# Kernel optimization log

Hardware: AMD Instinct MI355X
Metric: run time of the kernel (lower is better)

Reference implementation:

```python
import jax, jax.numpy as jnp
import numpy as np

B, E, N = 8, 256, 32          # triples, padded edges per triple, neighbors per edge
D, RD = 512, 768              # graph_dim, relation-semantic dim
R = 2000                      # num relations
L = 2                         # relation-context layers
K = 8                         # top_k neighbor similarity
M, HEADS = 32, 8              # memory tokens, memory-attention heads
HLLM = 4096                   # llm hidden size
EPS = 1e-5


def _ln(x, g, b):
    mu = jnp.mean(x, -1, keepdims=True)
    var = jnp.mean(jnp.square(x - mu), -1, keepdims=True)
    return (x - mu) * jax.lax.rsqrt(var + EPS) * g + b


def setup_inputs() -> dict:
    key = jax.random.key(0)
    ks = iter(jax.random.split(key, 40))
    nrm = lambda shape, s=0.02: jax.random.normal(next(ks), shape, jnp.float32) * s
    return {
        'edge_rel_ids': jax.random.randint(next(ks), (B, E), 0, R, jnp.int32),
        'neighbor_rel_ids': jax.random.randint(next(ks), (B, E, N), 0, R, jnp.int32),
        'edge_mask': jnp.ones((B, E), jnp.float32),
        'rel_emb': nrm((R, RD), 1.0),
        'rp_w': nrm((D, RD)), 'rp_b': jnp.zeros((D,), jnp.float32),
        'ly_vw': nrm((L, D, D)), 'ly_vb': jnp.zeros((L, D), jnp.float32),
        'ly_ow': nrm((L, D, D)), 'ly_ob': jnp.zeros((L, D), jnp.float32),
        'ly_n1g': jnp.ones((L, D), jnp.float32), 'ly_n1b': jnp.zeros((L, D), jnp.float32),
        'ly_n2g': jnp.ones((L, D), jnp.float32), 'ly_n2b': jnp.zeros((L, D), jnp.float32),
        'ly_w1': nrm((L, 4 * D, D)), 'ly_b1': jnp.zeros((L, 4 * D), jnp.float32),
        'ly_w2': nrm((L, D, 4 * D)), 'ly_b2': jnp.zeros((L, D), jnp.float32),
        'mem_q': nrm((M, D)),
        't_qw': nrm((D, D)), 't_qb': jnp.zeros((D,), jnp.float32),
        't_kw': nrm((D, D)), 't_kb': jnp.zeros((D,), jnp.float32),
        't_vw': nrm((D, D)), 't_vb': jnp.zeros((D,), jnp.float32),
        't_ow': nrm((D, D)), 't_ob': jnp.zeros((D,), jnp.float32),
        'proj_w': nrm((HLLM, D)), 'proj_b': jnp.zeros((HLLM,), jnp.float32),
    }


def reference(edge_rel_ids, neighbor_rel_ids, edge_mask, rel_emb, rp_w, rp_b,
              ly_vw, ly_vb, ly_ow, ly_ob, ly_n1g, ly_n1b, ly_n2g, ly_n2b,
              ly_w1, ly_b1, ly_w2, ly_b2, mem_q,
              t_qw, t_qb, t_kw, t_kb, t_vw, t_vb, t_ow, t_ob, proj_w, proj_b):
    rel_vector = lambda ids: rel_emb[ids] @ rp_w.T + rp_b  # embedding gather + rel_proj
    rel_vec = rel_vector(edge_rel_ids)            # [B,E,D]
    neigh = rel_vector(neighbor_rel_ids)          # [B,E,N,D] dominant gather traffic
    # per-edge cosine similarity to neighbor relations, top-k mean aggregation
    rn = rel_vec / jnp.maximum(jnp.linalg.norm(rel_vec, axis=-1, keepdims=True), 1e-12)
    nn_ = neigh / jnp.maximum(jnp.linalg.norm(neigh, axis=-1, keepdims=True), 1e-12)
    sims = jnp.einsum('bend,bed->ben', nn_, rn)   # [B,E,N]
    _, top_idx = jax.lax.top_k(sims, K)           # [B,E,K]
    agg = jnp.take_along_axis(neigh, top_idx[..., None], axis=2).mean(axis=2)  # [B,E,D]
    # RelationContextLayer stack. Each layer attends from one edge-state token to a
    # single context token: softmax over one key is identically 1, so the MHA
    # reduces exactly to out_proj(v_proj(context)) -- same math as torch MHA here.
    states = rel_vec
    for l in range(L):
        attn = (agg @ ly_vw[l].T + ly_vb[l]) @ ly_ow[l].T + ly_ob[l]
        states = _ln(states + attn, ly_n1g[l], ly_n1b[l])
        ff = jax.nn.gelu(states @ ly_w1[l].T + ly_b1[l], approximate=False) @ ly_w2[l].T + ly_b2[l]
        states = _ln(states + ff, ly_n2g[l], ly_n2b[l])
        states = states * edge_mask[..., None]
    # GraphMemoryTokenizer: learned queries cross-attend over padded edge states
    dh = D // HEADS
    q = (mem_q @ t_qw.T + t_qb).reshape(M, HEADS, dh)
    k = (states @ t_kw.T + t_kb).reshape(B, E, HEADS, dh)
    v = (states @ t_vw.T + t_vb).reshape(B, E, HEADS, dh)
    scores = jnp.einsum('mhd,behd->bhme', q, k) / jnp.sqrt(jnp.asarray(dh, q.dtype))
    scores = jnp.where(edge_mask[:, None, None, :] == 0, jnp.finfo(scores.dtype).min, scores)
    attnw = jax.nn.softmax(scores, axis=-1)
    mem = jnp.einsum('bhme,behd->bmhd', attnw, v).reshape(B, M, D)
    mem = mem @ t_ow.T + t_ob
    no_edges = jnp.sum(edge_mask, axis=1) == 0    # rows with zero edges -> zero memory
    mem = jnp.where(no_edges[:, None, None], 0.0, mem)
    return mem @ proj_w.T + proj_b                # [B,M,HLLM]
```

## Files before the change

kernel.cpp:

```cpp
#include <hip/hip_runtime.h>
#include <hip/hip_bf16.h>
#include <math.h>

#define B_   8
#define E_   256
#define N_   32
#define D_   512
#define RD_  768
#define R_   2000
#define L_   2
#define K_   8
#define M_   32
#define H_   8
#define DH_  64
#define HL_  4096

typedef float f32x4 __attribute__((ext_vector_type(4)));
typedef __bf16 bf16x8 __attribute__((ext_vector_type(8)));
typedef const __attribute__((address_space(1))) void GVoid;
typedef __attribute__((address_space(3))) void LVoid;

__device__ __forceinline__ float gelu_exact(float x) {
    return 0.5f * x * (1.0f + erff(x * 0.70710678118654752f));
}
__device__ __forceinline__ unsigned short f2bf(float x) {
    return __hip_bfloat16_raw(__float2bfloat16(x)).x;
}

template <int TM, int TN, int ACT_GELU, int OUT_BF16, int HAS_BIAS, int FLAGS>
__global__ __launch_bounds__(256) void gemm_mfma(const unsigned short* __restrict__ A,
                                                 const unsigned short* __restrict__ W,
                                                 const float* __restrict__ bias,
                                                 void* __restrict__ Cv,
                                                 int M, int N, int K,
                                                 size_t sA, size_t sW, size_t sC,
                                                 const float* __restrict__ rowflag) {
    constexpr int WTM = TM / 2, WTN = TN / 2;
    constexpr int RM = WTM / 16, RN = WTN / 16;
    constexpr int AI = TM / 32;
    constexpr int BI = TN / 32;
    __shared__ __align__(16) unsigned short As[TM * 64];
    __shared__ __align__(16) unsigned short Bs[TN * 64];

    const size_t z = blockIdx.z;
    A += z * sA; W += z * sW;

    const int tid = threadIdx.x;
    const int wave = tid >> 6, lane = tid & 63;
    const int quad = lane >> 4, l16 = lane & 15;
    const int wm = wave >> 1, wn = wave & 1;
    const int bm = blockIdx.y * TM, bn = blockIdx.x * TN;

    const int sub = lane >> 3;
    const int cpr = (lane & 7) ^ sub;

    f32x4 acc[RM][RN];
#pragma unroll
    for (int i = 0; i < RM; i++)
#pragma unroll
        for (int j = 0; j < RN; j++) acc[i][j] = (f32x4){0.f, 0.f, 0.f, 0.f};

    for (int k0 = 0; k0 < K; k0 += 64) {
        __syncthreads();
#pragma unroll
        for (int i = 0; i < AI; i++) {
            int r0 = (wave * AI + i) * 8;
            const unsigned short* g = A + (size_t)(bm + r0 + sub) * K + k0 + cpr * 8;
            __builtin_amdgcn_global_load_lds((GVoid*)g, (LVoid*)&As[r0 * 64], 16, 0, 0);
        }
#pragma unroll
        for (int i = 0; i < BI; i++) {
            int r0 = (wave * BI + i) * 8;
            const unsigned short* g = W + (size_t)(bn + r0 + sub) * K + k0 + cpr * 8;
            __builtin_amdgcn_global_load_lds((GVoid*)g, (LVoid*)&Bs[r0 * 64], 16, 0, 0);
        }
        __syncthreads();

#pragma unroll
        for (int h = 0; h < 2; h++) {
            bf16x8 af[RM], bf[RN];
#pragma unroll
            for (int i = 0; i < RM; i++) {
                int r = wm * WTM + i * 16 + l16;
                int ch = (h * 4 + quad) ^ (r & 7);
                af[i] = *(const bf16x8*)&As[r * 64 + ch * 8];
            }
#pragma unroll
            for (int j = 0; j < RN; j++) {
                int r = wn * WTN + j * 16 + l16;
                int ch = (h * 4 + quad) ^ (r & 7);
                bf[j] = *(const bf16x8*)&Bs[r * 64 + ch * 8];
            }
#pragma unroll
            for (int i = 0; i < RM; i++)
#pragma unroll
                for (int j = 0; j < RN; j++)
                    acc[i][j] = __builtin_amdgcn_mfma_f32_16x16x32_bf16(af[i], bf[j], acc[i][j], 0, 0, 0);
        }
    }

#pragma unroll
    for (int i = 0; i < RM; i++) {
#pragma unroll
        for (int j = 0; j < RN; j++) {
            int c = bn + wn * WTN + j * 16 + l16;
            float bv = HAS_BIAS ? bias[c] : 0.f;
#pragma unroll
            for (int reg = 0; reg < 4; reg++) {
                int r = bm + wm * WTM + i * 16 + quad * 4 + reg;
                if (r < M) {
                    float v = acc[i][j][reg] + bv;
                    if (ACT_GELU) v = gelu_exact(v);
                    if (FLAGS) v *= rowflag[r >> 5];
                    if (OUT_BF16)
                        ((unsigned short*)(Cv))[z * sC + (size_t)r * N + c] = f2bf(v);
                    else
                        ((float*)(Cv))[z * sC + (size_t)r * N + c] = v;
                }
            }
        }
    }
}

struct PrepArgs {
    const float* src[9];
    unsigned short* dst[9];
    int cum4[10];
    int nb_cvt, nb_tr, nb_bf, total4;
    const float* ly_vw; unsigned short* vwT;
    const float* ly_ow; const float* ly_vb; const float* ly_ob; float* bfuse;
    const float* t_kb; const float* t_vb; float* kvb;
    const float* edge_mask; float* flags;
    const float* mem_q; const float* t_qw; const float* t_qb; float* qbuf;
};

__global__ __launch_bounds__(256) void prep_all(PrepArgs a) {
    int bx = blockIdx.x, tid = threadIdx.x;
    if (bx < a.nb_cvt) {
        int i = bx * 256 + tid;
        if (i < a.total4) {
            int k = 0;
#pragma unroll
            for (int j = 0; j < 8; j++) if (i >= a.cum4[j + 1]) k = j + 1;
            int o = i - a.cum4[k];
            float4 v = ((const float4*)a.src[k])[o];
            ushort4 u;
            u.x = f2bf(v.x); u.y = f2bf(v.y); u.z = f2bf(v.z); u.w = f2bf(v.w);
            ((ushort4*)a.dst[k])[o] = u;
        }
        return;
    }
    bx -= a.nb_cvt;
    if (bx < a.nb_tr) {
        __shared__ float tile[32][33];
        int l = bx >> 8, t16 = bx & 255;
        int j0 = (t16 >> 4) * 32, k0 = (t16 & 15) * 32;
        int tx = tid & 31, ty = tid >> 5;
        const float* src = a.ly_vw + (size_t)l * 512 * 512;
        for (int r = ty; r < 32; r += 8)
            tile[r][tx] = src[(size_t)(j0 + r) * 512 + k0 + tx];
        __syncthreads();
        unsigned short* dst = a.vwT + (size_t)l * 512 * 512;
        for (int r = ty; r < 32; r += 8)
            dst[(size_t)(k0 + r) * 512 + j0 + tx] = f2bf(tile[tx][r]);
        return;
    }
    bx -= a.nb_tr;
    if (bx < a.nb_bf) {
        int wid = bx * 4 + (tid >> 6);
        int z = wid >> 9, n = wid & 511, lane = tid & 63;
        const float* owr = a.ly_ow + (size_t)z * 512 * 512 + (size_t)n * 512;
        const float* vbr = a.ly_vb + (size_t)z * 512;
        float s = 0.f;
#pragma unroll
        for (int j = 0; j < 8; j++) s += owr[lane + 64 * j] * vbr[lane + 64 * j];
#pragma unroll
        for (int off = 32; off; off >>= 1) s += __shfl_xor(s, off, 64);
        if (lane == 0) a.bfuse[z * 512 + n] = s + a.ly_ob[z * 512 + n];
        return;
    }
    bx -= a.nb_bf;
    if (bx < 1) {
        for (int n = tid; n < 512; n += 256) {
            a.kvb[n] = a.t_kb[n];
            a.kvb[n + 512] = a.t_vb[n];
        }
        __shared__ float red[4];
        for (int b = 0; b < B_; b++) {
            float s = a.edge_mask[b * E_ + tid];
#pragma unroll
            for (int off = 32; off; off >>= 1) s += __shfl_xor(s, off, 64);
            if ((tid & 63) == 0) red[tid >> 6] = s;
            __syncthreads();
            if (tid == 0)
                a.flags[b] = (red[0] + red[1] + red[2] + red[3] == 0.f) ? 0.f : 1.f;
            __syncthreads();
        }
        return;
    }
    bx -= 1;
    {
        int wid = bx * 4 + (tid >> 6);
        int m = wid >> 9, n = wid & 511, lane = tid & 63;
        const float* ar = a.mem_q + (size_t)m * 512;
        const float* br = a.t_qw + (size_t)n * 512;
        float s = 0.f;
#pragma unroll
        for (int j = 0; j < 8; j++) s += ar[lane + 64 * j] * br[lane + 64 * j];
#pragma unroll
        for (int off = 32; off; off >>= 1) s += __shfl_xor(s, off, 64);
        if (lane == 0) a.qbuf[(size_t)m * 512 + n] = s + a.t_qb[n];
    }
}

__global__ void sim_topk_agg(const int* __restrict__ eids, const int* __restrict__ nids,
                             const float* __restrict__ proj,
                             unsigned short* __restrict__ agg_bf, float* __restrict__ states) {
    int be = blockIdx.x, tid = threadIdx.x;
    __shared__ float ev[512];
    __shared__ float sims[32];
    __shared__ int nid_s[32];
    __shared__ int sel[8];

    int eid = eids[be];
    const float* ep = proj + (size_t)eid * D_;
    float e0 = ep[tid], e1 = ep[tid + 256];
    ev[tid] = e0; ev[tid + 256] = e1;
    states[(size_t)be * D_ + tid] = e0;
    states[(size_t)be * D_ + tid + 256] = e1;
    if (tid < 32) nid_s[tid] = nids[be * N_ + tid];
    __syncthreads();

    int wid = tid >> 6, lane = tid & 63;
    float se = 0.f;
#pragma unroll
    for (int j = 0; j < 8; j++) { float v = ev[lane + 64 * j]; se += v * v; }
#pragma unroll
    for (int off = 32; off; off >>= 1) se += __shfl_xor(se, off, 64);
    float en = fmaxf(sqrtf(se), 1e-12f);

    for (int n = wid; n < N_; n += 4) {
        int nid = nid_s[n];
        const float* np = proj + (size_t)nid * D_;
        float s = 0.f, s2 = 0.f;
#pragma unroll
        for (int j = 0; j < 8; j++) {
            float v = np[lane + 64 * j];
            s += v * ev[lane + 64 * j];
            s2 += v * v;
        }
#pragma unroll
        for (int off = 32; off; off >>= 1) {
            s += __shfl_xor(s, off, 64);
            s2 += __shfl_xor(s2, off, 64);
        }
        if (lane == 0) sims[n] = s / (fmaxf(sqrtf(s2), 1e-12f) * en);
    }
    __syncthreads();

    if (tid == 0) {
        unsigned used = 0;
        for (int k = 0; k < K_; k++) {
            float best = -3.402823466e38f; int bi = 0;
            for (int n = 0; n < N_; n++)
                if (!((used >> n) & 1u) && sims[n] > best) { best = sims[n]; bi = n; }
            used |= 1u << bi;
            sel[k] = nid_s[bi];
        }
    }
    __syncthreads();

    float a0 = 0.f, a1 = 0.f;
#pragma unroll
    for (int k = 0; k < K_; k++) {
        const float* sp = proj + (size_t)sel[k] * D_;
        a0 += sp[tid]; a1 += sp[tid + 256];
    }
    agg_bf[(size_t)be * D_ + tid] = f2bf(a0 * 0.125f);
    agg_bf[(size_t)be * D_ + tid + 256] = f2bf(a1 * 0.125f);
}

__global__ void add_ln_kernel(const float* __restrict__ x, const float* __restrict__ y,
                              int ystride, const float* __restrict__ g,
                              const float* __restrict__ bb, const float* __restrict__ mask,
                              float* __restrict__ out, unsigned short* __restrict__ out_bf) {
    int t = blockIdx.x, tid = threadIdx.x;
    const float* xr = x + (size_t)t * D_;
    const float* yr = y + (size_t)t * ystride;
    float x0 = xr[tid] + yr[tid];
    float x1 = xr[tid + 256] + yr[tid + 256];
    __shared__ float red[8];
    float s = x0 + x1;
#pragma unroll
    for (int off = 32; off; off >>= 1) s += __shfl_xor(s, off, 64);
    int wid = tid >> 6;
    if ((tid & 63) == 0) red[wid] = s;
    __syncthreads();
    float mean = (red[0] + red[1] + red[2] + red[3]) * (1.f / 512.f);
    float d0 = x0 - mean, d1 = x1 - mean;
    float v = d0 * d0 + d1 * d1;
#pragma unroll
    for (int off = 32; off; off >>= 1) v += __shfl_xor(v, off, 64);
    if ((tid & 63) == 0) red[4 + wid] = v;
    __syncthreads();
    float var = (red[4] + red[5] + red[6] + red[7]) * (1.f / 512.f);
    float rs = rsqrtf(var + 1e-5f);
    float mv = mask ? mask[t] : 1.f;
    float o0 = (d0 * rs * g[tid] + bb[tid]) * mv;
    float o1 = (d1 * rs * g[tid + 256] + bb[tid + 256]) * mv;
    out[(size_t)t * D_ + tid] = o0;
    out[(size_t)t * D_ + tid + 256] = o1;
    out_bf[(size_t)t * D_ + tid] = f2bf(o0);
    out_bf[(size_t)t * D_ + tid + 256] = f2bf(o1);
}

__global__ void mem_attn(const float* __restrict__ qb, const float* __restrict__ kv,
                         const float* __restrict__ mask, unsigned short* __restrict__ memb) {
    int idx = blockIdx.x;
    int b = idx & 7;
    int h = (idx >> 3) & 7;
    int m = idx >> 6;
    int tid = threadIdx.x;
    __shared__ float qh[64];
    __shared__ float sc[256];
    __shared__ float red[8];
    __shared__ float oacc[4][64];

    float mk = mask[b * E_ + tid];
    if (tid < 64) qh[tid] = qb[m * D_ + h * DH_ + tid];
    __syncthreads();
    const float* kr = kv + ((size_t)(b * E_ + tid)) * 1024 + h * DH_;
    float s = 0.f;
#pragma unroll
    for (int d = 0; d < DH_; d += 4) {
        float4 k4 = *(const float4*)(kr + d);
        s += k4.x * qh[d] + k4.y * qh[d + 1] + k4.z * qh[d + 2] + k4.w * qh[d + 3];
    }
    s *= 0.125f;
    if (mk == 0.f) s = -3.402823466e38f;
    float mx = s;
#pragma unroll
    for (int off = 32; off; off >>= 1) mx = fmaxf(mx, __shfl_xor(mx, off, 64));
    if ((tid & 63) == 0) red[tid >> 6] = mx;
    __syncthreads();
    mx = fmaxf(fmaxf(red[0], red[1]), fmaxf(red[2], red[3]));
    float p = expf(s - mx);
    float sum = p;
#pragma unroll
    for (int off = 32; off; off >>= 1) sum += __shfl_xor(sum, off, 64);
    if ((tid & 63) == 0) red[4 + (tid >> 6)] = sum;
    __syncthreads();
    sum = red[4] + red[5] + red[6] + red[7];
    sc[tid] = p / sum;
    __syncthreads();
    int d = tid & 63, part = tid >> 6;
    const float* vcol = kv + ((size_t)(b * E_ + part * 64)) * 1024 + 512 + h * DH_ + d;
    float acc = 0.f;
#pragma unroll 8
    for (int e = 0; e < 64; e++) acc += sc[part * 64 + e] * vcol[(size_t)e * 1024];
    oacc[part][d] = acc;
    __syncthreads();
    if (part == 0)
        memb[((size_t)(b * M_ + m)) * D_ + h * DH_ + d] =
            f2bf(oacc[0][d] + oacc[1][d] + oacc[2][d] + oacc[3][d]);
}

extern "C" void kernel_launch(void* const* d_in, const int* in_sizes, int n_in,
                              void* d_out, int out_size, void* d_ws, size_t ws_size,
                              hipStream_t stream) {
    const int*   edge_rel_ids     = (const int*)d_in[0];
    const int*   neighbor_rel_ids = (const int*)d_in[1];
    const float* edge_mask        = (const float*)d_in[2];
    const float* rel_emb          = (const float*)d_in[3];
    const float* rp_w             = (const float*)d_in[4];
    const float* rp_b             = (const float*)d_in[5];
    const float* ly_vw            = (const float*)d_in[6];
    const float* ly_vb            = (const float*)d_in[7];
    const float* ly_ow            = (const float*)d_in[8];
    const float* ly_ob            = (const float*)d_in[9];
    const float* ly_n1g           = (const float*)d_in[10];
    const float* ly_n1b           = (const float*)d_in[11];
    const float* ly_n2g           = (const float*)d_in[12];
    const float* ly_n2b           = (const float*)d_in[13];
    const float* ly_w1            = (const float*)d_in[14];
    const float* ly_b1            = (const float*)d_in[15];
    const float* ly_w2            = (const float*)d_in[16];
    const float* ly_b2            = (const float*)d_in[17];
    const float* mem_q            = (const float*)d_in[18];
    const float* t_qw             = (const float*)d_in[19];
    const float* t_qb             = (const float*)d_in[20];
    const float* t_kw             = (const float*)d_in[21];
    const float* t_kb             = (const float*)d_in[22];
    const float* t_vw             = (const float*)d_in[23];
    const float* t_vb             = (const float*)d_in[24];
    const float* t_ow             = (const float*)d_in[25];
    const float* t_ob             = (const float*)d_in[26];
    const float* proj_w           = (const float*)d_in[27];
    const float* proj_b           = (const float*)d_in[28];
    float* out = (float*)d_out;
    (void)ws_size; (void)in_sizes; (void)n_in; (void)out_size;

    char* ws = (char*)d_ws;
    size_t off = 0;
    auto allocf = [&](size_t n) { float* p = (float*)(ws + off); off += ((n * 4 + 255) & ~(size_t)255); return p; };
    auto allocb = [&](size_t n) { unsigned short* p = (unsigned short*)(ws + off); off += ((n * 2 + 255) & ~(size_t)255); return p; };

    const int T = B_ * E_;

    float* proj    = allocf((size_t)R_ * D_);
    float* states  = allocf((size_t)T * D_);
    float* tmpB    = allocf((size_t)T * D_);
    float* attnall = allocf((size_t)T * 2 * D_);
    float* qbuf    = allocf((size_t)M_ * D_);
    float* bfuse   = allocf(2 * D_);
    float* kvb     = allocf(2 * D_);
    float* flags   = allocf(B_);
    float* kvbuf   = attnall;

    unsigned short* rel_bf    = allocb((size_t)2048 * RD_);
    unsigned short* rpw_bf    = allocb((size_t)D_ * RD_);
    unsigned short* agg_bf    = allocb((size_t)T * D_);
    unsigned short* states_bf = allocb((size_t)T * D_);
    unsigned short* ff1_bf    = allocb((size_t)T * 4 * D_);
    unsigned short* vwT_bf    = allocb((size_t)L_ * D_ * D_);
    unsigned short* ow_bf     = allocb((size_t)L_ * D_ * D_);
    unsigned short* wfuse_bf  = allocb((size_t)L_ * D_ * D_);
    unsigned short* w1_bf     = allocb((size_t)L_ * 4 * D_ * D_);
    unsigned short* w2_bf     = allocb((size_t)L_ * 4 * D_ * D_);
    unsigned short* kvw_bf    = allocb((size_t)2 * D_ * D_);
    unsigned short* tow_bf    = allocb((size_t)D_ * D_);
    unsigned short* pw_bf     = allocb((size_t)HL_ * D_);
    unsigned short* memb_bf   = allocb((size_t)B_ * M_ * D_);
    unsigned short* mem2_bf   = allocb((size_t)B_ * M_ * D_);

    PrepArgs a;
    int sizes[9] = { R_ * RD_, D_ * RD_, L_ * D_ * D_, L_ * 4 * D_ * D_,
                     L_ * 4 * D_ * D_, D_ * D_, D_ * D_, D_ * D_, HL_ * D_ };
    const float* srcs[9] = { rel_emb, rp_w, ly_ow, ly_w1, ly_w2, t_kw, t_vw, t_ow, proj_w };
    unsigned short* dsts[9] = { rel_bf, rpw_bf, ow_bf, w1_bf, w2_bf,
                                kvw_bf, kvw_bf + (size_t)D_ * D_, tow_bf, pw_bf };
    int cum = 0;
    for (int i = 0; i < 9; i++) {
        a.src[i] = srcs[i]; a.dst[i] = dsts[i];
        a.cum4[i] = cum; cum += sizes[i] / 4;
    }
    a.cum4[9] = cum;
    a.total4 = cum;
    a.nb_cvt = (cum + 255) / 256;
    a.nb_tr = 512;
    a.nb_bf = 256;
    a.ly_vw = ly_vw; a.vwT = vwT_bf;
    a.ly_ow = ly_ow; a.ly_vb = ly_vb; a.ly_ob = ly_ob; a.bfuse = bfuse;
    a.t_kb = t_kb; a.t_vb = t_vb; a.kvb = kvb;
    a.edge_mask = edge_mask; a.flags = flags;
    a.mem_q = mem_q; a.t_qw = t_qw; a.t_qb = t_qb; a.qbuf = qbuf;
    int nblk = a.nb_cvt + a.nb_tr + a.nb_bf + 1 + 4096;
    prep_all<<<nblk, 256, 0, stream>>>(a);

    gemm_mfma<32, 64, 0, 0, 1, 0><<<dim3(D_ / 64, 64), 256, 0, stream>>>(
        rel_bf, rpw_bf, rp_b, proj, R_, D_, RD_, 0, 0, 0, nullptr);
    sim_topk_agg<<<T, 256, 0, stream>>>(edge_rel_ids, neighbor_rel_ids, proj,
                                        agg_bf, states);

    gemm_mfma<32, 64, 0, 1, 0, 0><<<dim3(8, 16, 2), 256, 0, stream>>>(
        ow_bf, vwT_bf, nullptr, wfuse_bf, D_, D_, D_,
        (size_t)D_ * D_, (size_t)D_ * D_, (size_t)D_ * D_, nullptr);
    gemm_mfma<64, 64, 0, 0, 1, 0><<<dim3(2 * D_ / 64, T / 64), 256, 0, stream>>>(
        agg_bf, wfuse_bf, bfuse, attnall, T, 2 * D_, D_, 0, 0, 0, nullptr);

    for (int l = 0; l < L_; l++) {
        add_ln_kernel<<<T, 256, 0, stream>>>(states, attnall + (size_t)l * D_, 2 * D_,
                                             ly_n1g + l * D_, ly_n1b + l * D_, nullptr,
                                             states, states_bf);
        gemm_mfma<64, 64, 1, 1, 1, 0><<<dim3(4 * D_ / 64, T / 64), 256, 0, stream>>>(
            states_bf, w1_bf + (size_t)l * 4 * D_ * D_, ly_b1 + l * 4 * D_,
            ff1_bf, T, 4 * D_, D_, 0, 0, 0, nullptr);
        gemm_mfma<32, 64, 0, 0, 1, 0><<<dim3(D_ / 64, T / 32), 256, 0, stream>>>(
            ff1_bf, w2_bf + (size_t)l * 4 * D_ * D_, ly_b2 + l * D_,
            tmpB, T, D_, 4 * D_, 0, 0, 0, nullptr);
        add_ln_kernel<<<T, 256, 0, stream>>>(states, tmpB, D_,
                                             ly_n2g + l * D_, ly_n2b + l * D_, edge_mask,
                                             states, states_bf);
    }

    gemm_mfma<64, 64, 0, 0, 1, 0><<<dim3(2 * D_ / 64, T / 64), 256, 0, stream>>>(
        states_bf, kvw_bf, kvb, kvbuf, T, 2 * D_, D_, 0, 0, 0, nullptr);

    mem_attn<<<B_ * M_ * H_, 256, 0, stream>>>(qbuf, kvbuf, edge_mask, memb_bf);

    gemm_mfma<32, 64, 0, 1, 1, 1><<<dim3(D_ / 64, 8), 256, 0, stream>>>(
        memb_bf, tow_bf, t_ob, mem2_bf, B_ * M_, D_, D_, 0, 0, 0, flags);

    gemm_mfma<32, 64, 0, 0, 1, 0><<<dim3(HL_ / 64, 8), 256, 0, stream>>>(
        mem2_bf, pw_bf, proj_b, out, B_ * M_, HL_, D_, 0, 0, 0, nullptr);
}
```

Before: 322.1 us.

## Fuse all stages into one persistent cooperative kernel with grid syncs

```diff
diff --git a/kernel.cpp b/kernel.cpp
--- a/kernel.cpp
+++ b/kernel.cpp
@@ -1,6 +1,9 @@
 #include <hip/hip_runtime.h>
+#include <hip/hip_cooperative_groups.h>
 #include <hip/hip_bf16.h>
 #include <math.h>
+
+namespace cg = cooperative_groups;
 
 #define B_   8
 #define E_   256
@@ -27,115 +30,130 @@
     return __hip_bfloat16_raw(__float2bfloat16(x)).x;
 }
 
-template <int TM, int TN, int ACT_GELU, int OUT_BF16, int HAS_BIAS, int FLAGS>
-__global__ __launch_bounds__(256) void gemm_mfma(const unsigned short* __restrict__ A,
-                                                 const unsigned short* __restrict__ W,
-                                                 const float* __restrict__ bias,
-                                                 void* __restrict__ Cv,
-                                                 int M, int N, int K,
-                                                 size_t sA, size_t sW, size_t sC,
-                                                 const float* __restrict__ rowflag) {
-    constexpr int WTM = TM / 2, WTN = TN / 2;
-    constexpr int RM = WTM / 16, RN = WTN / 16;
-    constexpr int AI = TM / 32;
-    constexpr int BI = TN / 32;
-    __shared__ __align__(16) unsigned short As[TM * 64];
-    __shared__ __align__(16) unsigned short Bs[TN * 64];
-
-    const size_t z = blockIdx.z;
-    A += z * sA; W += z * sW;
-
-    const int tid = threadIdx.x;
-    const int wave = tid >> 6, lane = tid & 63;
-    const int quad = lane >> 4, l16 = lane & 15;
-    const int wm = wave >> 1, wn = wave & 1;
-    const int bm = blockIdx.y * TM, bn = blockIdx.x * TN;
-
-    const int sub = lane >> 3;
-    const int cpr = (lane & 7) ^ sub;
-
-    f32x4 acc[RM][RN];
-#pragma unroll
-    for (int i = 0; i < RM; i++)
-#pragma unroll
-        for (int j = 0; j < RN; j++) acc[i][j] = (f32x4){0.f, 0.f, 0.f, 0.f};
-
-    for (int k0 = 0; k0 < K; k0 += 64) {
-        __syncthreads();
-#pragma unroll
-        for (int i = 0; i < AI; i++) {
-            int r0 = (wave * AI + i) * 8;
-            const unsigned short* g = A + (size_t)(bm + r0 + sub) * K + k0 + cpr * 8;
-            __builtin_amdgcn_global_load_lds((GVoid*)g, (LVoid*)&As[r0 * 64], 16, 0, 0);
-        }
-#pragma unroll
-        for (int i = 0; i < BI; i++) {
-            int r0 = (wave * BI + i) * 8;
-            const unsigned short* g = W + (size_t)(bn + r0 + sub) * K + k0 + cpr * 8;
-            __builtin_amdgcn_global_load_lds((GVoid*)g, (LVoid*)&Bs[r0 * 64], 16, 0, 0);
-        }
-        __syncthreads();
-
-#pragma unroll
-        for (int h = 0; h < 2; h++) {
-            bf16x8 af[RM], bf[RN];
-#pragma unroll
-            for (int i = 0; i < RM; i++) {
-                int r = wm * WTM + i * 16 + l16;
-                int ch = (h * 4 + quad) ^ (r & 7);
-                af[i] = *(const bf16x8*)&As[r * 64 + ch * 8];
-            }
-#pragma unroll
-            for (int j = 0; j < RN; j++) {
-                int r = wn * WTN + j * 16 + l16;
-                int ch = (h * 4 + quad) ^ (r & 7);
-                bf[j] = *(const bf16x8*)&Bs[r * 64 + ch * 8];
-            }
-#pragma unroll
-            for (int i = 0; i < RM; i++)
-#pragma unroll
-                for (int j = 0; j < RN; j++)
-                    acc[i][j] = __builtin_amdgcn_mfma_f32_16x16x32_bf16(af[i], bf[j], acc[i][j], 0, 0, 0);
-        }
-    }
-
-#pragma unroll
-    for (int i = 0; i < RM; i++) {
-#pragma unroll
-        for (int j = 0; j < RN; j++) {
-            int c = bn + wn * WTN + j * 16 + l16;
-            float bv = HAS_BIAS ? bias[c] : 0.f;
-#pragma unroll
-            for (int reg = 0; reg < 4; reg++) {
-                int r = bm + wm * WTM + i * 16 + quad * 4 + reg;
-                if (r < M) {
-                    float v = acc[i][j][reg] + bv;
-                    if (ACT_GELU) v = gelu_exact(v);
-                    if (FLAGS) v *= rowflag[r >> 5];
-                    if (OUT_BF16)
-                        ((unsigned short*)(Cv))[z * sC + (size_t)r * N + c] = f2bf(v);
-                    else
-                        ((float*)(Cv))[z * sC + (size_t)r * N + c] = v;
-                }
-            }
-        }
-    }
-}
-
-struct PrepArgs {
-    const float* src[9];
-    unsigned short* dst[9];
-    int cum4[10];
-    int nb_cvt, nb_tr, nb_bf, total4;
+struct AllArgs {
+    const float* csrc[9]; unsigned short* cdst[9]; int cum4[10];
+    int nb_cvt, total4, nb_prep;
     const float* ly_vw; unsigned short* vwT;
     const float* ly_ow; const float* ly_vb; const float* ly_ob; float* bfuse;
     const float* t_kb; const float* t_vb; float* kvb;
     const float* edge_mask; float* flags;
     const float* mem_q; const float* t_qw; const float* t_qb; float* qbuf;
+    const int* eids; const int* nids;
+    unsigned short* rel_bf; unsigned short* rpw_bf; const float* rp_b; float* proj;
+    unsigned short* agg_bf; float* states; unsigned short* states_bf;
+    unsigned short* ow_bf; unsigned short* wfuse;
+    float* attnall;
+    const float* n1g; const float* n1b; const float* n2g; const float* n2b;
+    unsigned short* w1; const float* b1; unsigned short* w2; const float* b2;
+    unsigned short* ff1; float* tmpB;
+    unsigned short* kvw; float* kvbuf;
+    unsigned short* membf; unsigned short* toww; const float* t_ob; unsigned short* mem2;
+    unsigned short* pw; const float* proj_b; float* outp;
 };
 
-__global__ __launch_bounds__(256) void prep_all(PrepArgs a) {
-    int bx = blockIdx.x, tid = threadIdx.x;
+template <int TM, int TN, int GELU_, int OBF_, int BIAS_, int FLAGS_>
+__device__ __forceinline__ void gemm_stage(const unsigned short* __restrict__ A,
+                                           const unsigned short* __restrict__ W,
+                                           const float* __restrict__ bias,
+                                           void* __restrict__ Cv,
+                                           int M, int N, int K,
+                                           const float* __restrict__ rowflag,
+                                           int zn, size_t sA, size_t sW, size_t sC,
+                                           unsigned char* SM) {
+    constexpr int WTM = TM / 2, WTN = TN / 2;
+    constexpr int RM = WTM / 16, RN = WTN / 16;
+    constexpr int AI = TM / 32, BI = TN / 32;
+    unsigned short* As = (unsigned short*)SM;
+    unsigned short* Bs = (unsigned short*)(SM + 8192);
+
+    const int tid = threadIdx.x;
+    const int wave = tid >> 6, lane = tid & 63;
+    const int quad = lane >> 4, l16 = lane & 15;
+    const int wm = wave >> 1, wn = wave & 1;
+    const int sub = lane >> 3;
+    const int cpr = (lane & 7) ^ sub;
+    const int ntx = N / TN;
+    const int nty = (M + TM - 1) / TM;
+    const int ntiles = ntx * nty * zn;
+
+    for (int t0 = blockIdx.x; t0 < ntiles; t0 += gridDim.x) {
+        int z = t0 / (ntx * nty);
+        int tt = t0 - z * (ntx * nty);
+        int bn = (tt % ntx) * TN, bm = (tt / ntx) * TM;
+        const unsigned short* Az = A + (size_t)z * sA;
+        const unsigned short* Wz = W + (size_t)z * sW;
+
+        f32x4 acc[RM][RN];
+#pragma unroll
+        for (int i = 0; i < RM; i++)
+#pragma unroll
+            for (int j = 0; j < RN; j++) acc[i][j] = (f32x4){0.f, 0.f, 0.f, 0.f};
+
+        for (int k0 = 0; k0 < K; k0 += 64) {
+            __syncthreads();
+#pragma unroll
+            for (int i = 0; i < AI; i++) {
+                int r0 = (wave * AI + i) * 8;
+                const unsigned short* g = Az + (size_t)(bm + r0 + sub) * K + k0 + cpr * 8;
+                __builtin_amdgcn_global_load_lds((GVoid*)g, (LVoid*)&As[r0 * 64], 16, 0, 0);
+            }
+#pragma unroll
+            for (int i = 0; i < BI; i++) {
+                int r0 = (wave * BI + i) * 8;
+                const unsigned short* g = Wz + (size_t)(bn + r0 + sub) * K + k0 + cpr * 8;
+                __builtin_amdgcn_global_load_lds((GVoid*)g, (LVoid*)&Bs[r0 * 64], 16, 0, 0);
+            }
+            __syncthreads();
+
+#pragma unroll
+            for (int h = 0; h < 2; h++) {
+                bf16x8 af[RM], bf[RN];
+#pragma unroll
+                for (int i = 0; i < RM; i++) {
+                    int r = wm * WTM + i * 16 + l16;
+                    int ch = (h * 4 + quad) ^ (r & 7);
+                    af[i] = *(const bf16x8*)&As[r * 64 + ch * 8];
+                }
+#pragma unroll
+                for (int j = 0; j < RN; j++) {
+                    int r = wn * WTN + j * 16 + l16;
+                    int ch = (h * 4 + quad) ^ (r & 7);
+                    bf[j] = *(const bf16x8*)&Bs[r * 64 + ch * 8];
+                }
+#pragma unroll
+                for (int i = 0; i < RM; i++)
+#pragma unroll
+                    for (int j = 0; j < RN; j++)
+                        acc[i][j] = __builtin_amdgcn_mfma_f32_16x16x32_bf16(af[i], bf[j], acc[i][j], 0, 0, 0);
+            }
+        }
+
+#pragma unroll
+        for (int i = 0; i < RM; i++) {
+#pragma unroll
+            for (int j = 0; j < RN; j++) {
+                int c = bn + wn * WTN + j * 16 + l16;
+                float bv = BIAS_ ? bias[c] : 0.f;
+#pragma unroll
+                for (int reg = 0; reg < 4; reg++) {
+                    int r = bm + wm * WTM + i * 16 + quad * 4 + reg;
+                    if (r < M) {
+                        float v = acc[i][j][reg] + bv;
+                        if (GELU_) v = gelu_exact(v);
+                        if (FLAGS_) v *= rowflag[r >> 5];
+                        if (OBF_)
+                            ((unsigned short*)Cv)[(size_t)z * sC + (size_t)r * N + c] = f2bf(v);
+                        else
+                            ((float*)Cv)[(size_t)z * sC + (size_t)r * N + c] = v;
+                    }
+                }
+            }
+        }
+    }
+}
+
+__device__ __forceinline__ void prep_unit(const AllArgs& a, int bx, unsigned char* SM) {
+    int tid = threadIdx.x;
     if (bx < a.nb_cvt) {
         int i = bx * 256 + tid;
         if (i < a.total4) {
@@ -143,30 +161,30 @@
 #pragma unroll
             for (int j = 0; j < 8; j++) if (i >= a.cum4[j + 1]) k = j + 1;
             int o = i - a.cum4[k];
-            float4 v = ((const float4*)a.src[k])[o];
+            float4 v = ((const float4*)a.csrc[k])[o];
             ushort4 u;
             u.x = f2bf(v.x); u.y = f2bf(v.y); u.z = f2bf(v.z); u.w = f2bf(v.w);
-            ((ushort4*)a.dst[k])[o] = u;
+            ((ushort4*)a.cdst[k])[o] = u;
         }
         return;
     }
     bx -= a.nb_cvt;
-    if (bx < a.nb_tr) {
-        __shared__ float tile[32][33];
+    if (bx < 512) {
+        float* tile = (float*)SM;
         int l = bx >> 8, t16 = bx & 255;
         int j0 = (t16 >> 4) * 32, k0 = (t16 & 15) * 32;
         int tx = tid & 31, ty = tid >> 5;
         const float* src = a.ly_vw + (size_t)l * 512 * 512;
         for (int r = ty; r < 32; r += 8)
-            tile[r][tx] = src[(size_t)(j0 + r) * 512 + k0 + tx];
+            tile[r * 33 + tx] = src[(size_t)(j0 + r) * 512 + k0 + tx];
         __syncthreads();
         unsigned short* dst = a.vwT + (size_t)l * 512 * 512;
         for (int r = ty; r < 32; r += 8)
-            dst[(size_t)(k0 + r) * 512 + j0 + tx] = f2bf(tile[tx][r]);
+            dst[(size_t)(k0 + r) * 512 + j0 + tx] = f2bf(tile[tx * 33 + r]);
         return;
     }
-    bx -= a.nb_tr;
-    if (bx < a.nb_bf) {
+    bx -= 512;
+    if (bx < 256) {
         int wid = bx * 4 + (tid >> 6);
         int z = wid >> 9, n = wid & 511, lane = tid & 63;
         const float* owr = a.ly_ow + (size_t)z * 512 * 512 + (size_t)n * 512;
@@ -179,13 +197,13 @@
         if (lane == 0) a.bfuse[z * 512 + n] = s + a.ly_ob[z * 512 + n];
         return;
     }
-    bx -= a.nb_bf;
+    bx -= 256;
     if (bx < 1) {
+        float* red = (float*)SM;
         for (int n = tid; n < 512; n += 256) {
             a.kvb[n] = a.t_kb[n];
             a.kvb[n + 512] = a.t_vb[n];
         }
-        __shared__ float red[4];
         for (int b = 0; b < B_; b++) {
             float s = a.edge_mask[b * E_ + tid];
 #pragma unroll
@@ -213,22 +231,20 @@
     }
 }
 
-__global__ void sim_topk_agg(const int* __restrict__ eids, const int* __restrict__ nids,
-                             const float* __restrict__ proj,
-                             unsigned short* __restrict__ agg_bf, float* __restrict__ states) {
-    int be = blockIdx.x, tid = threadIdx.x;
-    __shared__ float ev[512];
-    __shared__ float sims[32];
-    __shared__ int nid_s[32];
-    __shared__ int sel[8];
-
-    int eid = eids[be];
-    const float* ep = proj + (size_t)eid * D_;
+__device__ __forceinline__ void topk_unit(const AllArgs& a, int be, unsigned char* SM) {
+    int tid = threadIdx.x;
+    float* ev = (float*)SM;
+    float* sims = (float*)(SM + 2048);
+    int* nid_s = (int*)(SM + 2176);
+    int* sel = (int*)(SM + 2304);
+
+    int eid = a.eids[be];
+    const float* ep = a.proj + (size_t)eid * D_;
     float e0 = ep[tid], e1 = ep[tid + 256];
     ev[tid] = e0; ev[tid + 256] = e1;
-    states[(size_t)be * D_ + tid] = e0;
-    states[(size_t)be * D_ + tid + 256] = e1;
-    if (tid < 32) nid_s[tid] = nids[be * N_ + tid];
+    a.states[(size_t)be * D_ + tid] = e0;
+    a.states[(size_t)be * D_ + tid + 256] = e1;
+    if (tid < 32) nid_s[tid] = a.nids[be * N_ + tid];
     __syncthreads();
 
     int wid = tid >> 6, lane = tid & 63;
@@ -241,7 +257,7 @@
 
     for (int n = wid; n < N_; n += 4) {
         int nid = nid_s[n];
-        const float* np = proj + (size_t)nid * D_;
+        const float* np = a.proj + (size_t)nid * D_;
         float s = 0.f, s2 = 0.f;
 #pragma unroll
         for (int j = 0; j < 8; j++) {
@@ -273,96 +289,179 @@
     float a0 = 0.f, a1 = 0.f;
 #pragma unroll
     for (int k = 0; k < K_; k++) {
-        const float* sp = proj + (size_t)sel[k] * D_;
+        const float* sp = a.proj + (size_t)sel[k] * D_;
         a0 += sp[tid]; a1 += sp[tid + 256];
     }
-    agg_bf[(size_t)be * D_ + tid] = f2bf(a0 * 0.125f);
-    agg_bf[(size_t)be * D_ + tid + 256] = f2bf(a1 * 0.125f);
-}
-
-__global__ void add_ln_kernel(const float* __restrict__ x, const float* __restrict__ y,
-                              int ystride, const float* __restrict__ g,
-                              const float* __restrict__ bb, const float* __restrict__ mask,
-                              float* __restrict__ out, unsigned short* __restrict__ out_bf) {
-    int t = blockIdx.x, tid = threadIdx.x;
-    const float* xr = x + (size_t)t * D_;
-    const float* yr = y + (size_t)t * ystride;
-    float x0 = xr[tid] + yr[tid];
-    float x1 = xr[tid + 256] + yr[tid + 256];
-    __shared__ float red[8];
-    float s = x0 + x1;
-#pragma unroll
-    for (int off = 32; off; off >>= 1) s += __shfl_xor(s, off, 64);
-    int wid = tid >> 6;
-    if ((tid & 63) == 0) red[wid] = s;
-    __syncthreads();
-    float mean = (red[0] + red[1] + red[2] + red[3]) * (1.f / 512.f);
-    float d0 = x0 - mean, d1 = x1 - mean;
-    float v = d0 * d0 + d1 * d1;
-#pragma unroll
-    for (int off = 32; off; off >>= 1) v += __shfl_xor(v, off, 64);
-    if ((tid & 63) == 0) red[4 + wid] = v;
-    __syncthreads();
-    float var = (red[4] + red[5] + red[6] + red[7]) * (1.f / 512.f);
-    float rs = rsqrtf(var + 1e-5f);
-    float mv = mask ? mask[t] : 1.f;
-    float o0 = (d0 * rs * g[tid] + bb[tid]) * mv;
-    float o1 = (d1 * rs * g[tid + 256] + bb[tid + 256]) * mv;
-    out[(size_t)t * D_ + tid] = o0;
-    out[(size_t)t * D_ + tid + 256] = o1;
-    out_bf[(size_t)t * D_ + tid] = f2bf(o0);
-    out_bf[(size_t)t * D_ + tid + 256] = f2bf(o1);
-}
-
-__global__ void mem_attn(const float* __restrict__ qb, const float* __restrict__ kv,
-                         const float* __restrict__ mask, unsigned short* __restrict__ memb) {
-    int idx = blockIdx.x;
-    int b = idx & 7;
-    int h = (idx >> 3) & 7;
-    int m = idx >> 6;
+    a.agg_bf[(size_t)be * D_ + tid] = f2bf(a0 * 0.125f);
+    a.agg_bf[(size_t)be * D_ + tid + 256] = f2bf(a1 * 0.125f);
+}
+
+__device__ __forceinline__ void add_ln_rows(const float* x, const float* y, int ystride,
+                                            const float* g, const float* bb,
+                                            const float* mask, float* out,
+                                            unsigned short* out_bf, unsigned char* SM) {
     int tid = threadIdx.x;
-    __shared__ float qh[64];
-    __shared__ float sc[256];
-    __shared__ float red[8];
-    __shared__ float oacc[4][64];
-
-    float mk = mask[b * E_ + tid];
-    if (tid < 64) qh[tid] = qb[m * D_ + h * DH_ + tid];
-    __syncthreads();
-    const float* kr = kv + ((size_t)(b * E_ + tid)) * 1024 + h * DH_;
-    float s = 0.f;
-#pragma unroll
-    for (int d = 0; d < DH_; d += 4) {
-        float4 k4 = *(const float4*)(kr + d);
-        s += k4.x * qh[d] + k4.y * qh[d + 1] + k4.z * qh[d + 2] + k4.w * qh[d + 3];
-    }
-    s *= 0.125f;
-    if (mk == 0.f) s = -3.402823466e38f;
-    float mx = s;
-#pragma unroll
-    for (int off = 32; off; off >>= 1) mx = fmaxf(mx, __shfl_xor(mx, off, 64));
-    if ((tid & 63) == 0) red[tid >> 6] = mx;
-    __syncthreads();
-    mx = fmaxf(fmaxf(red[0], red[1]), fmaxf(red[2], red[3]));
-    float p = expf(s - mx);
-    float sum = p;
-#pragma unroll
-    for (int off = 32; off; off >>= 1) sum += __shfl_xor(sum, off, 64);
-    if ((tid & 63) == 0) red[4 + (tid >> 6)] = sum;
-    __syncthreads();
-    sum = red[4] + red[5] + red[6] + red[7];
-    sc[tid] = p / sum;
-    __syncthreads();
-    int d = tid & 63, part = tid >> 6;
-    const float* vcol = kv + ((size_t)(b * E_ + part * 64)) * 1024 + 512 + h * DH_ + d;
-    float acc = 0.f;
+    float* red = (float*)SM;
+    for (int t = blockIdx.x; t < B_ * E_; t += gridDim.x) {
+        const float* xr = x + (size_t)t * D_;
+        const float* yr = y + (size_t)t * ystride;
+        float x0 = xr[tid] + yr[tid];
+        float x1 = xr[tid + 256] + yr[tid + 256];
+        float s = x0 + x1;
+#pragma unroll
+        for (int off = 32; off; off >>= 1) s += __shfl_xor(s, off, 64);
+        int wid = tid >> 6;
+        if ((tid & 63) == 0) red[wid] = s;
+        __syncthreads();
+        float mean = (red[0] + red[1] + red[2] + red[3]) * (1.f / 512.f);
+        float d0 = x0 - mean, d1 = x1 - mean;
+        float v = d0 * d0 + d1 * d1;
+#pragma unroll
+        for (int off = 32; off; off >>= 1) v += __shfl_xor(v, off, 64);
+        if ((tid & 63) == 0) red[4 + wid] = v;
+        __syncthreads();
+        float var = (red[4] + red[5] + red[6] + red[7]) * (1.f / 512.f);
+        float rs = rsqrtf(var + 1e-5f);
+        float mv = mask ? mask[t] : 1.f;
+        float o0 = (d0 * rs * g[tid] + bb[tid]) * mv;
+        float o1 = (d1 * rs * g[tid + 256] + bb[tid + 256]) * mv;
+        out[(size_t)t * D_ + tid] = o0;
+        out[(size_t)t * D_ + tid + 256] = o1;
+        out_bf[(size_t)t * D_ + tid] = f2bf(o0);
+        out_bf[(size_t)t * D_ + tid + 256] = f2bf(o1);
+        __syncthreads();
+    }
+}
+
+__device__ __forceinline__ void mem_attn_units(const AllArgs& a, unsigned char* SM) {
+    int tid = threadIdx.x;
+    float* qh = (float*)SM;
+    float* sc = (float*)(SM + 256);
+    float* red = (float*)(SM + 1280);
+    float* oacc = (float*)(SM + 1344);
+    for (int idx = blockIdx.x; idx < B_ * M_ * H_; idx += gridDim.x) {
+        __syncthreads();
+        int b = idx & 7;
+        int h = (idx >> 3) & 7;
+        int m = idx >> 6;
+        float mk = a.edge_mask[b * E_ + tid];
+        if (tid < 64) qh[tid] = a.qbuf[m * D_ + h * DH_ + tid];
+        __syncthreads();
+        const float* kr = a.kvbuf + ((size_t)(b * E_ + tid)) * 1024 + h * DH_;
+        float s = 0.f;
+#pragma unroll
+        for (int d = 0; d < DH_; d += 4) {
+            float4 k4 = *(const float4*)(kr + d);
+            s += k4.x * qh[d] + k4.y * qh[d + 1] + k4.z * qh[d + 2] + k4.w * qh[d + 3];
+        }
+        s *= 0.125f;
+        if (mk == 0.f) s = -3.402823466e38f;
+        float mx = s;
+#pragma unroll
+        for (int off = 32; off; off >>= 1) mx = fmaxf(mx, __shfl_xor(mx, off, 64));
+        if ((tid & 63) == 0) red[tid >> 6] = mx;
+        __syncthreads();
+        mx = fmaxf(fmaxf(red[0], red[1]), fmaxf(red[2], red[3]));
+        float p = expf(s - mx);
+        float sum = p;
+#pragma unroll
+        for (int off = 32; off; off >>= 1) sum += __shfl_xor(sum, off, 64);
+        if ((tid & 63) == 0) red[4 + (tid >> 6)] = sum;
+        __syncthreads();
+        sum = red[4] + red[5] + red[6] + red[7];
+        sc[tid] = p / sum;
+        __syncthreads();
+        int d = tid & 63, part = tid >> 6;
+        const float* vcol = a.kvbuf + ((size_t)(b * E_ + part * 64)) * 1024 + 512 + h * DH_ + d;
+        float acc = 0.f;
 #pragma unroll 8
-    for (int e = 0; e < 64; e++) acc += sc[part * 64 + e] * vcol[(size_t)e * 1024];
-    oacc[part][d] = acc;
-    __syncthreads();
-    if (part == 0)
-        memb[((size_t)(b * M_ + m)) * D_ + h * DH_ + d] =
-            f2bf(oacc[0][d] + oacc[1][d] + oacc[2][d] + oacc[3][d]);
+        for (int e = 0; e < 64; e++) acc += sc[part * 64 + e] * vcol[(size_t)e * 1024];
+        oacc[part * 64 + d] = acc;
+        __syncthreads();
+        if (part == 0)
+            a.membf[((size_t)(b * M_ + m)) * D_ + h * DH_ + d] =
+                f2bf(oacc[d] + oacc[64 + d] + oacc[128 + d] + oacc[192 + d]);
+    }
+}
+
+__device__ __forceinline__ void run_stage(const AllArgs& a, int s, unsigned char* SM) {
+    switch (s) {
+    case 0:
+        for (int u = blockIdx.x; u < a.nb_prep; u += gridDim.x) {
+            __syncthreads();
+            prep_unit(a, u, SM);
+        }
+        break;
+    case 1:
+        gemm_stage<32, 64, 0, 0, 1, 0>(a.rel_bf, a.rpw_bf, a.rp_b, a.proj,
+                                       R_, D_, RD_, nullptr, 1, 0, 0, 0, SM);
+        break;
+    case 2:
+        for (int u = blockIdx.x; u < B_ * E_; u += gridDim.x) {
+            __syncthreads();
+            topk_unit(a, u, SM);
+        }
+        gemm_stage<32, 64, 0, 1, 0, 0>(a.ow_bf, a.vwT, nullptr, a.wfuse,
+                                       D_, D_, D_, nullptr, 2,
+                                       (size_t)D_ * D_, (size_t)D_ * D_, (size_t)D_ * D_, SM);
+        break;
+    case 3:
+        gemm_stage<64, 64, 0, 0, 1, 0>(a.agg_bf, a.wfuse, a.bfuse, a.attnall,
+                                       B_ * E_, 2 * D_, D_, nullptr, 1, 0, 0, 0, SM);
+        break;
+    case 4: case 8: {
+        int l = (s - 4) / 4;
+        add_ln_rows(a.states, a.attnall + (size_t)l * D_, 2 * D_,
+                    a.n1g + l * D_, a.n1b + l * D_, nullptr,
+                    a.states, a.states_bf, SM);
+        break;
+    }
+    case 5: case 9: {
+        int l = (s - 4) / 4;
+        gemm_stage<64, 64, 1, 1, 1, 0>(a.states_bf, a.w1 + (size_t)l * 4 * D_ * D_,
+                                       a.b1 + l * 4 * D_, a.ff1,
+                                       B_ * E_, 4 * D_, D_, nullptr, 1, 0, 0, 0, SM);
+        break;
+    }
+    case 6: case 10: {
+        int l = (s - 4) / 4;
+        gemm_stage<32, 64, 0, 0, 1, 0>(a.ff1, a.w2 + (size_t)l * 4 * D_ * D_,
+                                       a.b2 + l * D_, a.tmpB,
+                                       B_ * E_, D_, 4 * D_, nullptr, 1, 0, 0, 0, SM);
+        break;
+    }
+    case 7: case 11: {
+        int l = (s - 4) / 4;
+        add_ln_rows(a.states, a.tmpB, D_,
+                    a.n2g + l * D_, a.n2b + l * D_, a.edge_mask,
+                    a.states, a.states_bf, SM);
+        break;
+    }
+    case 12:
+        gemm_stage<64, 64, 0, 0, 1, 0>(a.states_bf, a.kvw, a.kvb, a.kvbuf,
+                                       B_ * E_, 2 * D_, D_, nullptr, 1, 0, 0, 0, SM);
+        break;
+    case 13:
+        mem_attn_units(a, SM);
+        break;
+    case 14:
+        gemm_stage<32, 64, 0, 1, 1, 1>(a.membf, a.toww, a.t_ob, a.mem2,
+                                       B_ * M_, D_, D_, a.flags, 1, 0, 0, 0, SM);
+        break;
+    case 15:
+        gemm_stage<32, 64, 0, 0, 1, 0>(a.mem2, a.pw, a.proj_b, a.outp,
+                                       B_ * M_, HL_, D_, nullptr, 1, 0, 0, 0, SM);
+        break;
+    }
+}
+
+__global__ __launch_bounds__(256, 2) void fused_all(AllArgs a, int s0, int s1) {
+    __shared__ __align__(16) unsigned char SM[16896];
+    cg::grid_group grid = cg::this_grid();
+    for (int s = s0; s < s1; s++) {
+        if (s > s0) grid.sync();
+        run_stage(a, s, SM);
+    }
 }
 
 extern "C" void kernel_launch(void* const* d_in, const int* in_sizes, int n_in,
@@ -397,7 +496,6 @@
     const float* t_ob             = (const float*)d_in[26];
     const float* proj_w           = (const float*)d_in[27];
     const float* proj_b           = (const float*)d_in[28];
-    float* out = (float*)d_out;
     (void)ws_size; (void)in_sizes; (void)n_in; (void)out_size;
 
     char* ws = (char*)d_ws;
@@ -433,7 +531,7 @@
     unsigned short* memb_bf   = allocb((size_t)B_ * M_ * D_);
     unsigned short* mem2_bf   = allocb((size_t)B_ * M_ * D_);
 
-    PrepArgs a;
+    AllArgs a;
     int sizes[9] = { R_ * RD_, D_ * RD_, L_ * D_ * D_, L_ * 4 * D_ * D_,
                      L_ * 4 * D_ * D_, D_ * D_, D_ * D_, D_ * D_, HL_ * D_ };
     const float* srcs[9] = { rel_emb, rp_w, ly_ow, ly_w1, ly_w2, t_kw, t_vw, t_ow, proj_w };
@@ -441,56 +539,36 @@
                                 kvw_bf, kvw_bf + (size_t)D_ * D_, tow_bf, pw_bf };
     int cum = 0;
     for (int i = 0; i < 9; i++) {
-        a.src[i] = srcs[i]; a.dst[i] = dsts[i];
+        a.csrc[i] = srcs[i]; a.cdst[i] = dsts[i];
         a.cum4[i] = cum; cum += sizes[i] / 4;
     }
     a.cum4[9] = cum;
     a.total4 = cum;
     a.nb_cvt = (cum + 255) / 256;
-    a.nb_tr = 512;
-    a.nb_bf = 256;
+    a.nb_prep = a.nb_cvt + 512 + 256 + 1 + 4096;
     a.ly_vw = ly_vw; a.vwT = vwT_bf;
     a.ly_ow = ly_ow; a.ly_vb = ly_vb; a.ly_ob = ly_ob; a.bfuse = bfuse;
     a.t_kb = t_kb; a.t_vb = t_vb; a.kvb = kvb;
     a.edge_mask = edge_mask; a.flags = flags;
     a.mem_q = mem_q; a.t_qw = t_qw; a.t_qb = t_qb; a.qbuf = qbuf;
-    int nblk = a.nb_cvt + a.nb_tr + a.nb_bf + 1 + 4096;
-    prep_all<<<nblk, 256, 0, stream>>>(a);
-
-    gemm_mfma<32, 64, 0, 0, 1, 0><<<dim3(D_ / 64, 64), 256, 0, stream>>>(
-        rel_bf, rpw_bf, rp_b, proj, R_, D_, RD_, 0, 0, 0, nullptr);
-    sim_topk_agg<<<T, 256, 0, stream>>>(edge_rel_ids, neighbor_rel_ids, proj,
-                                        agg_bf, states);
-
-    gemm_mfma<32, 64, 0, 1, 0, 0><<<dim3(8, 16, 2), 256, 0, stream>>>(
-        ow_bf, vwT_bf, nullptr, wfuse_bf, D_, D_, D_,
-        (size_t)D_ * D_, (size_t)D_ * D_, (size_t)D_ * D_, nullptr);
-    gemm_mfma<64, 64, 0, 0, 1, 0><<<dim3(2 * D_ / 64, T / 64), 256, 0, stream>>>(
-        agg_bf, wfuse_bf, bfuse, attnall, T, 2 * D_, D_, 0, 0, 0, nullptr);
-
-    for (int l = 0; l < L_; l++) {
-        add_ln_kernel<<<T, 256, 0, stream>>>(states, attnall + (size_t)l * D_, 2 * D_,
-                                             ly_n1g + l * D_, ly_n1b + l * D_, nullptr,
-                                             states, states_bf);
-        gemm_mfma<64, 64, 1, 1, 1, 0><<<dim3(4 * D_ / 64, T / 64), 256, 0, stream>>>(
-            states_bf, w1_bf + (size_t)l * 4 * D_ * D_, ly_b1 + l * 4 * D_,
-            ff1_bf, T, 4 * D_, D_, 0, 0, 0, nullptr);
-        gemm_mfma<32, 64, 0, 0, 1, 0><<<dim3(D_ / 64, T / 32), 256, 0, stream>>>(
-            ff1_bf, w2_bf + (size_t)l * 4 * D_ * D_, ly_b2 + l * D_,
-            tmpB, T, D_, 4 * D_, 0, 0, 0, nullptr);
-        add_ln_kernel<<<T, 256, 0, stream>>>(states, tmpB, D_,
-                                             ly_n2g + l * D_, ly_n2b + l * D_, edge_mask,
-                                             states, states_bf);
-    }
-
-    gemm_mfma<64, 64, 0, 0, 1, 0><<<dim3(2 * D_ / 64, T / 64), 256, 0, stream>>>(
-        states_bf, kvw_bf, kvb, kvbuf, T, 2 * D_, D_, 0, 0, 0, nullptr);
-
-    mem_attn<<<B_ * M_ * H_, 256, 0, stream>>>(qbuf, kvbuf, edge_mask, memb_bf);
-
-    gemm_mfma<32, 64, 0, 1, 1, 1><<<dim3(D_ / 64, 8), 256, 0, stream>>>(
-        memb_bf, tow_bf, t_ob, mem2_bf, B_ * M_, D_, D_, 0, 0, 0, flags);
-
-    gemm_mfma<32, 64, 0, 0, 1, 0><<<dim3(HL_ / 64, 8), 256, 0, stream>>>(
-        mem2_bf, pw_bf, proj_b, out, B_ * M_, HL_, D_, 0, 0, 0, nullptr);
-}
+    a.eids = edge_rel_ids; a.nids = neighbor_rel_ids;
+    a.rel_bf = rel_bf; a.rpw_bf = rpw_bf; a.rp_b = rp_b; a.proj = proj;
+    a.agg_bf = agg_bf; a.states = states; a.states_bf = states_bf;
+    a.ow_bf = ow_bf; a.wfuse = wfuse_bf;
+    a.attnall = attnall;
+    a.n1g = ly_n1g; a.n1b = ly_n1b; a.n2g = ly_n2g; a.n2b = ly_n2b;
+    a.w1 = w1_bf; a.b1 = ly_b1; a.w2 = w2_bf; a.b2 = ly_b2;
+    a.ff1 = ff1_bf; a.tmpB = tmpB;
+    a.kvw = kvw_bf; a.kvbuf = kvbuf;
+    a.membf = memb_bf; a.toww = tow_bf; a.t_ob = t_ob; a.mem2 = mem2_bf;
+    a.pw = pw_bf; a.proj_b = proj_b; a.outp = (float*)d_out;
+
+    int s0 = 0, s1 = 16;
+    void* kargs[] = { (void*)&a, (void*)&s0, (void*)&s1 };
+    hipError_t err = hipLaunchCooperativeKernel((void*)fused_all, dim3(512), dim3(256),
+                                                kargs, 0, stream);
+    if (err != hipSuccess) {
+        for (int s = 0; s < 16; s++)
+            fused_all<<<512, 256, 0, stream>>>(a, s, s + 1);
+    }
+}
```

Result: slower. 1.234 ms (+283.3%).
